# Optimization experiments

Measured on AMD Instinct MI355X. Metric: run time of the kernel, lower is better.

## Reference

```python
import jax, jax.numpy as jnp
import numpy as np

D_MODEL = 512
N_HEADS = 8
D_HEAD = D_MODEL // N_HEADS


def entmax15(z, axis=-1):
    """Exact sort-based entmax-1.5 along `axis` (Peters et al. 2019)."""
    z = jnp.moveaxis(z, axis, -1)
    x = z / 2.0
    x = x - jnp.max(x, axis=-1, keepdims=True)
    x_srt = -jnp.sort(-x, axis=-1)  # descending
    D = x_srt.shape[-1]
    k = jnp.arange(1, D + 1, dtype=x.dtype)
    cs = jnp.cumsum(x_srt, axis=-1)
    cs2 = jnp.cumsum(x_srt * x_srt, axis=-1)
    mean = cs / k
    ss = k * (cs2 / k - mean * mean)
    delta = (1.0 - ss) / k
    tau = mean - jnp.sqrt(jnp.clip(delta, 0.0))
    support = (tau <= x_srt).astype(jnp.int32)
    support_size = jnp.sum(support, axis=-1, keepdims=True)  # >= 1
    tau_star = jnp.take_along_axis(tau, support_size - 1, axis=-1)
    out = jnp.square(jnp.clip(x - tau_star, 0.0))
    return jnp.moveaxis(out, -1, axis)


def setup_inputs() -> dict:
    key = jax.random.key(0)
    ks = jax.random.split(key, 12)
    B, L = 8, 1024
    s = 1.0 / np.sqrt(D_MODEL)
    inp = {
        "query": jax.random.normal(ks[0], (B, L, D_MODEL), jnp.float32),
        "key": jax.random.normal(ks[1], (B, L, D_MODEL), jnp.float32),
        "value": jax.random.normal(ks[2], (B, L, D_MODEL), jnp.float32),
        "key_padding_mask": jnp.zeros((B, L), jnp.bool_),
        "q_w": jax.random.uniform(ks[3], (D_MODEL, D_MODEL), jnp.float32, -s, s),
        "q_b": jax.random.uniform(ks[4], (D_MODEL,), jnp.float32, -s, s),
        "k_w": jax.random.uniform(ks[5], (D_MODEL, D_MODEL), jnp.float32, -s, s),
        "k_b": jax.random.uniform(ks[6], (D_MODEL,), jnp.float32, -s, s),
        "v_w": jax.random.uniform(ks[7], (D_MODEL, D_MODEL), jnp.float32, -s, s),
        "v_b": jax.random.uniform(ks[8], (D_MODEL,), jnp.float32, -s, s),
        "out_w": jax.random.uniform(ks[9], (D_MODEL, D_MODEL), jnp.float32, -s, s),
        "out_b": jax.random.uniform(ks[10], (D_MODEL,), jnp.float32, -s, s),
    }
    return inp


def reference(query, key, value, key_padding_mask, q_w, q_b, k_w, k_b, v_w, v_b, out_w, out_b):
    B, L, _ = query.shape
    scale = D_HEAD ** -0.5
    # torch Linear: y = x @ W^T + b
    def split_heads(x):
        return x.reshape(B, L, N_HEADS, D_HEAD).transpose(0, 2, 1, 3)  # [B,H,L,d]
    q = split_heads(query @ q_w.T + q_b)
    k = split_heads(key @ k_w.T + k_b)
    v = split_heads(value @ v_w.T + v_b)
    scores = jnp.einsum('bhqd,bhkd->bhqk', q, k) * scale  # [B,H,L,L]
    mask = key_padding_mask[:, None, None, :]
    scores = jnp.where(mask, jnp.asarray(-1e9, scores.dtype), scores)
    attn = entmax15(scores, axis=-1)  # dropout in eval mode -> identity
    ctx = jnp.einsum('bhqk,bhkd->bhqd', attn, v)
    ctx = ctx.transpose(0, 2, 1, 3).reshape(B, L, D_MODEL)
    return ctx @ out_w.T + out_b
```

## Files before the change

kernel.cpp:

```cpp
#include <hip/hip_runtime.h>
#include <stdint.h>

typedef _Float16 f16;
typedef __attribute__((ext_vector_type(8))) f16 f16x8;
typedef __attribute__((ext_vector_type(2))) f16 h2;
typedef __attribute__((ext_vector_type(4))) float f32x4;
typedef unsigned short u16;
typedef unsigned int u32;
typedef unsigned char u8;

#define LL 1024
#define DM 512

__device__ __forceinline__ u16 f2h(float f){ return __builtin_bit_cast(u16, (f16)f); }
__device__ __forceinline__ u32 pack2(float a, float b){
  h2 v; v.x = (f16)a; v.y = (f16)b; return __builtin_bit_cast(u32, v);
}
__device__ __forceinline__ f32x4 mfma16h(f16x8 a, f16x8 b, f32x4 c){
  return __builtin_amdgcn_mfma_f32_16x16x32_f16(a, b, c, 0, 0, 0);
}

template<int CTRL>
__device__ __forceinline__ float dpp_mov(float x){
  return __builtin_bit_cast(float,
    __builtin_amdgcn_update_dpp(0, __builtin_bit_cast(int, x), CTRL, 0xF, 0xF, true));
}
__device__ __forceinline__ float red_add16(float v){
  v += dpp_mov<0x128>(v);
  v += dpp_mov<0x124>(v);
  v += dpp_mov<0x122>(v);
  v += dpp_mov<0x121>(v);
  return v;
}
__device__ __forceinline__ float red_max16(float v){
  v = fmaxf(v, dpp_mov<0x128>(v));
  v = fmaxf(v, dpp_mov<0x124>(v));
  v = fmaxf(v, dpp_mov<0x122>(v));
  v = fmaxf(v, dpp_mov<0x121>(v));
  return v;
}

struct CvtArgs {
  const float* src[7];
  u16* dst[7];
  int n4[7];
};

__global__ __launch_bounds__(256) void cvt_kernel(CvtArgs a){
  int seg = blockIdx.y;
  const float4* s = (const float4*)a.src[seg];
  ushort4* d = (ushort4*)a.dst[seg];
  int n4 = a.n4[seg];
  for (int i = blockIdx.x*blockDim.x + threadIdx.x; i < n4; i += gridDim.x*blockDim.x){
    float4 v = s[i];
    ushort4 o;
    o.x = f2h(v.x); o.y = f2h(v.y); o.z = f2h(v.z); o.w = f2h(v.w);
    d[i] = o;
  }
}

struct QkvArgs {
  const u16* A[3];
  const u16* W[3];
  const float* bias[3];
  u16* dst[3];
  float scale[3];
};

__global__ __launch_bounds__(256,2) void proj_qkv(QkvArgs args){
  __shared__ u16 SM[128*128];
  u16* As = SM;
  u16* Bs = SM + 128*64;
  const int tid = threadIdx.x;
  const int w = tid>>6, lane = tid&63;
  const int g = lane>>4, r16 = lane&15;
  const int wr = w>>1, wc = w&1;

  const int which = blockIdx.y>>2, nt = blockIdx.y&3;
  const bool isV = (which==2);
  const u16* A = args.A[which];
  const u16* W = args.W[which];
  const float* bias = args.bias[which];
  u16* dsth = args.dst[which];
  const float scale = args.scale[which];

  const int m0 = blockIdx.x*128, n0 = nt*128;

  f32x4 acc[4][4] = {};

  int rowc[4], slc[4];
  #pragma unroll
  for (int i=0;i<4;++i){
    int c = i*256+tid;
    rowc[i] = c>>3;
    slc[i] = (c&7) ^ ((c>>3)&7);
  }

  const int fswz = r16 & 7;

  for (int k0=0; k0<DM; k0+=64){
    #pragma unroll
    for (int i=0;i<4;++i){
      int c = i*256+tid;
      __builtin_amdgcn_global_load_lds(
        (const __attribute__((address_space(1))) void*)(A + (size_t)(m0+rowc[i])*DM + k0 + slc[i]*8),
        (__attribute__((address_space(3))) void*)(&As[c*8]), 16, 0, 0);
      __builtin_amdgcn_global_load_lds(
        (const __attribute__((address_space(1))) void*)(W + (size_t)(n0+rowc[i])*DM + k0 + slc[i]*8),
        (__attribute__((address_space(3))) void*)(&Bs[c*8]), 16, 0, 0);
    }
    __syncthreads();

    f16x8 af[4][2], bfr[4][2];
    #pragma unroll
    for (int mi=0; mi<4; ++mi){
      int row = wr*64 + mi*16 + r16;
      #pragma unroll
      for (int ks=0; ks<2; ++ks)
        af[mi][ks] = *(const f16x8*)(&As[row*64 + ((ks*4+g)^fswz)*8]);
    }
    #pragma unroll
    for (int ni=0; ni<4; ++ni){
      int row = wc*64 + ni*16 + r16;
      #pragma unroll
      for (int ks=0; ks<2; ++ks)
        bfr[ni][ks] = *(const f16x8*)(&Bs[row*64 + ((ks*4+g)^fswz)*8]);
    }
    if (isV){
      #pragma unroll
      for (int mi=0; mi<4; ++mi)
        #pragma unroll
        for (int ni=0; ni<4; ++ni){
          acc[mi][ni] = mfma16h(af[mi][0], bfr[ni][0], acc[mi][ni]);
          acc[mi][ni] = mfma16h(af[mi][1], bfr[ni][1], acc[mi][ni]);
        }
    } else {
      #pragma unroll
      for (int mi=0; mi<4; ++mi)
        #pragma unroll
        for (int ni=0; ni<4; ++ni){
          acc[mi][ni] = mfma16h(bfr[ni][0], af[mi][0], acc[mi][ni]);
          acc[mi][ni] = mfma16h(bfr[ni][1], af[mi][1], acc[mi][ni]);
        }
    }
    __syncthreads();
  }

  if (!isV){
    #pragma unroll
    for (int mi=0; mi<4; ++mi){
      #pragma unroll
      for (int ni=0; ni<4; ++ni){
        f32x4 a = acc[mi][ni];
        int row = wr*64 + mi*16 + r16;
        int c   = wc*16 + ni*4 + g;
        float4 bv = *(const float4*)(bias + n0 + c*4);
        uint2 pk;
        pk.x = pack2((a[0]+bv.x)*scale, (a[1]+bv.y)*scale);
        pk.y = pack2((a[2]+bv.z)*scale, (a[3]+bv.w)*scale);
        *(uint2*)(&SM[row*128 + ((c ^ ((row&7)<<2))<<2)]) = pk;
      }
    }
  } else {
    #pragma unroll
    for (int mi=0; mi<4; ++mi){
      #pragma unroll
      for (int ni=0; ni<4; ++ni){
        f32x4 a = acc[mi][ni];
        int fl = wc*64 + ni*16 + r16;
        int kc = wr*16 + mi*4 + g;
        float bv = bias[n0 + fl];
        uint2 pk;
        pk.x = pack2(a[0]+bv, a[1]+bv);
        pk.y = pack2(a[2]+bv, a[3]+bv);
        *(uint2*)(&SM[fl*128 + ((kc ^ ((fl&7)<<2))<<2)]) = pk;
      }
    }
  }
  __syncthreads();

  #pragma unroll
  for (int rr=0; rr<8; ++rr){
    int row = w*32 + rr*4 + (lane>>4);
    int c0 = (lane&15)*2;
    int cs = c0 ^ ((row&7)<<2);
    uint4 v = *(const uint4*)(&SM[row*128 + (cs<<2)]);
    if (!isV){
      *(uint4*)(dsth + (size_t)(m0+row)*DM + n0 + (c0<<2)) = v;
    } else {
      int n = n0 + row;
      int hh = n>>6, d = n&63, bb = m0>>10;
      *(uint4*)(dsth + (size_t)((bb*8+hh)*64 + d)*1024 + (m0&1023) + (c0<<2)) = v;
    }
  }
}

__global__ __launch_bounds__(256,2) void proj_out(
    const u16* __restrict__ A, const u16* __restrict__ W,
    const float* __restrict__ bias, float* __restrict__ dstf)
{
  __shared__ u16 As[64*64];
  __shared__ u16 Bs[128*64];
  const int tid = threadIdx.x;
  const int w = tid>>6, lane = tid&63;
  const int g = lane>>4, r16 = lane&15;
  const int m0 = blockIdx.x*64, n0 = blockIdx.y*128;

  f32x4 acc[4][2] = {};

  int rowa[2], slota[2];
  #pragma unroll
  for (int i=0;i<2;++i){ int c = i*256+tid; rowa[i]=c>>3; slota[i]=c&7; }
  int rowb[4], slotb[4];
  #pragma unroll
  for (int i=0;i<4;++i){ int c = i*256+tid; rowb[i]=c>>3; slotb[i]=c&7; }

  uint4 ra[2], rb[4];
  #pragma unroll
  for (int i=0;i<2;++i)
    ra[i] = *(const uint4*)(A + (size_t)(m0+rowa[i])*DM + slota[i]*8);
  #pragma unroll
  for (int i=0;i<4;++i)
    rb[i] = *(const uint4*)(W + (size_t)(n0+rowb[i])*DM + slotb[i]*8);

  const int fswz = r16 & 7;

  for (int k0=0; k0<DM; k0+=64){
    __syncthreads();
    #pragma unroll
    for (int i=0;i<2;++i)
      *(uint4*)(&As[rowa[i]*64 + (slota[i]^(rowa[i]&7))*8]) = ra[i];
    #pragma unroll
    for (int i=0;i<4;++i)
      *(uint4*)(&Bs[rowb[i]*64 + (slotb[i]^(rowb[i]&7))*8]) = rb[i];
    __syncthreads();
    int kn = (k0+64 < DM) ? (k0+64) : 0;
    #pragma unroll
    for (int i=0;i<2;++i)
      ra[i] = *(const uint4*)(A + (size_t)(m0+rowa[i])*DM + kn + slota[i]*8);
    #pragma unroll
    for (int i=0;i<4;++i)
      rb[i] = *(const uint4*)(W + (size_t)(n0+rowb[i])*DM + kn + slotb[i]*8);

    f16x8 af[4][2], bfr[2][2];
    #pragma unroll
    for (int mi=0; mi<4; ++mi){
      int row = mi*16 + r16;
      #pragma unroll
      for (int ks=0; ks<2; ++ks)
        af[mi][ks] = *(const f16x8*)(&As[row*64 + ((ks*4+g)^fswz)*8]);
    }
    #pragma unroll
    for (int ni=0; ni<2; ++ni){
      int row = w*32 + ni*16 + r16;
      #pragma unroll
      for (int ks=0; ks<2; ++ks)
        bfr[ni][ks] = *(const f16x8*)(&Bs[row*64 + ((ks*4+g)^fswz)*8]);
    }
    #pragma unroll
    for (int mi=0; mi<4; ++mi)
      #pragma unroll
      for (int ni=0; ni<2; ++ni){
        acc[mi][ni] = mfma16h(bfr[ni][0], af[mi][0], acc[mi][ni]);
        acc[mi][ni] = mfma16h(bfr[ni][1], af[mi][1], acc[mi][ni]);
      }
  }

  #pragma unroll
  for (int mi=0; mi<4; ++mi){
    #pragma unroll
    for (int ni=0; ni<2; ++ni){
      int m  = m0 + mi*16 + r16;
      int nb = n0 + w*32 + ni*16 + g*4;
      float4 bv = *(const float4*)(bias + nb);
      float4 o;
      o.x = acc[mi][ni][0]+bv.x; o.y = acc[mi][ni][1]+bv.y;
      o.z = acc[mi][ni][2]+bv.z; o.w = acc[mi][ni][3]+bv.w;
      *(float4*)(dstf + (size_t)m*DM + nb) = o;
    }
  }
}

__global__ __launch_bounds__(256,4) void attn_entmax(
    const u16* __restrict__ Qf, const u16* __restrict__ Kf,
    const u16* __restrict__ Vt, const u8* __restrict__ mask,
    u16* __restrict__ ctx)
{
  __shared__ u16 S[16*1024];

  const int tid = threadIdx.x, w = tid>>6, lane = tid&63;
  const int g = lane>>4, r16 = lane&15;
  const int bid = blockIdx.x;
  const int bh = ((bid&7)<<3) | ((bid>>3)&7);
  const int qb = bid>>6;
  const int b = bh>>3, h = bh&7;
  const int q0 = qb*16;
  const u16* Qb = Qf + ((size_t)(b*LL + q0))*DM + h*64;
  const u16* Kb = Kf + ((size_t)(b*LL))*DM + h*64;

  f16x8 qf0 = *(const f16x8*)(Qb + (size_t)r16*DM + g*8);
  f16x8 qf1 = *(const f16x8*)(Qb + (size_t)r16*DM + 32 + g*8);
  #pragma unroll
  for (int kt=0; kt<16; ++kt){
    int krow = w*256 + kt*16;
    const u16* kp = Kb + (size_t)(krow + r16)*DM + g*8;
    f16x8 kf0 = *(const f16x8*)(kp);
    f16x8 kf1 = *(const f16x8*)(kp + 32);
    f32x4 acc = {};
    acc = mfma16h(kf0, qf0, acc);
    acc = mfma16h(kf1, qf1, acc);
    int kb = krow + g*4;
    u32 m4 = *(const u32*)(mask + b*LL + kb);
    float v0 = (m4 & 0xFFu)       ? -30000.f : acc[0];
    float v1 = (m4 & 0xFF00u)     ? -30000.f : acc[1];
    float v2 = (m4 & 0xFF0000u)   ? -30000.f : acc[2];
    float v3 = (m4 & 0xFF000000u) ? -30000.f : acc[3];
    int cc = ((kb>>6)&7) ^ (r16&7);
    uint2 pk; pk.x = pack2(v0,v1); pk.y = pack2(v2,v3);
    *(uint2*)(&S[r16*LL + (kb ^ (cc<<3))]) = pk;
  }
  __syncthreads();

  {
    const int r = w*4 + g;
    const int ccb = (r16 ^ r) & 7;
    h2 zp[32];
    #pragma unroll
    for (int c=0;c<8;++c){
      uint4 v = *(const uint4*)(&S[r*LL + ((r16*64 + c*8) ^ (ccb<<3))]);
      zp[c*4+0] = __builtin_bit_cast(h2, v.x);
      zp[c*4+1] = __builtin_bit_cast(h2, v.y);
      zp[c*4+2] = __builtin_bit_cast(h2, v.z);
      zp[c*4+3] = __builtin_bit_cast(h2, v.w);
    }
    h2 m2 = zp[0];
    #pragma unroll
    for (int t=1;t<32;++t) m2 = __builtin_elementwise_max(m2, zp[t]);
    float mx = red_max16(fmaxf((float)m2.x, (float)m2.y));

    const h2 zero2 = (h2)(f16)0;
    float lo = mx - 1.0f, hi = mx, tau = mx - 0.5f;
    #pragma unroll 1
    for (int it=0; it<6; ++it){
      f16 th = (f16)tau;
      h2 t2; t2.x = th; t2.y = th;
      h2 s1a = zero2, s1b = zero2, s2a = zero2, s2b = zero2;
      #pragma unroll
      for (int t=0;t<32;t+=2){
        h2 d0 = __builtin_elementwise_max(zp[t]   - t2, zero2);
        h2 d1 = __builtin_elementwise_max(zp[t+1] - t2, zero2);
        s1a = s1a + d0;        s1b = s1b + d1;
        s2a = s2a + d0*d0;     s2b = s2b + d1*d1;
      }
      h2 s1h = s1a + s1b, s2h = s2a + s2b;
      float s1 = red_add16((float)s1h.x + (float)s1h.y);
      float s2 = red_add16((float)s2h.x + (float)s2h.y);
      if (s2 >= 1.0f) lo = tau; else hi = tau;
      float tn = tau + (s2 - 1.0f)/(2.0f*s1);
      tau = (tn >= lo && tn < hi) ? tn : 0.5f*(lo+hi);
    }

    {
      f16 th = (f16)tau;
      h2 t2; t2.x = th; t2.y = th;
      h2 psa = zero2, psb = zero2;
      #pragma unroll
      for (int t=0;t<32;t+=2){
        h2 d0 = __builtin_elementwise_max(zp[t]   - t2, zero2);
        h2 d1 = __builtin_elementwise_max(zp[t+1] - t2, zero2);
        h2 p0 = d0*d0, p1 = d1*d1;
        zp[t] = p0; zp[t+1] = p1;
        psa = psa + p0; psb = psb + p1;
      }
      h2 ps2 = psa + psb;
      float ps = red_add16((float)ps2.x + (float)ps2.y);
      f16 iv = (f16)(1.0f/ps);
      h2 i2; i2.x = iv; i2.y = iv;
      #pragma unroll
      for (int c=0;c<8;++c){
        uint4 v;
        v.x = __builtin_bit_cast(u32, (h2)(zp[c*4+0]*i2));
        v.y = __builtin_bit_cast(u32, (h2)(zp[c*4+1]*i2));
        v.z = __builtin_bit_cast(u32, (h2)(zp[c*4+2]*i2));
        v.w = __builtin_bit_cast(u32, (h2)(zp[c*4+3]*i2));
        *(uint4*)(&S[r*LL + ((r16*64 + c*8) ^ (ccb<<3))]) = v;
      }
    }
  }
  __syncthreads();

  const u16* vrow = Vt + (size_t)(bh*64 + w*16 + r16)*LL;
  f32x4 o0 = {}, o1 = {};
  const int prow = r16;
  #pragma unroll 8
  for (int kt=0; kt<32; ++kt){
    int k = kt*32 + g*8;
    int cc = ((k>>6)&7) ^ (prow&7);
    f16x8 pa = *(const f16x8*)(&S[prow*LL + (k ^ (cc<<3))]);
    f16x8 vb = *(const f16x8*)(vrow + k);
    if (kt & 1) o1 = mfma16h(pa, vb, o1);
    else        o0 = mfma16h(pa, vb, o0);
  }
  #pragma unroll
  for (int r=0;r<4;++r){
    int q = q0 + g*4 + r;
    ctx[(size_t)(b*LL + q)*DM + h*64 + w*16 + r16] = f2h(o0[r] + o1[r]);
  }
}

extern "C" void kernel_launch(void* const* d_in, const int* in_sizes, int n_in,
                              void* d_out, int out_size, void* d_ws, size_t ws_size,
                              hipStream_t stream) {
  const float* query = (const float*)d_in[0];
  const float* key   = (const float*)d_in[1];
  const float* value = (const float*)d_in[2];
  const u8*    maskp = (const u8*)d_in[3];
  const float* q_w = (const float*)d_in[4];
  const float* q_b = (const float*)d_in[5];
  const float* k_w = (const float*)d_in[6];
  const float* k_b = (const float*)d_in[7];
  const float* v_w = (const float*)d_in[8];
  const float* v_b = (const float*)d_in[9];
  const float* out_w = (const float*)d_in[10];
  const float* out_b = (const float*)d_in[11];
  float* out = (float*)d_out;

  u16* qx = (u16*)d_ws;
  u16* kx = qx + 4194304;
  u16* vx = kx + 4194304;
  u16* wq = vx + 4194304;
  u16* wk = wq + 262144;
  u16* wv = wk + 262144;
  u16* wo = wv + 262144;
  u16* Qbuf = wo + 262144;
  u16* Kbuf = Qbuf + 4194304;
  u16* Vt   = Kbuf + 4194304;
  u16* ctxb = Vt + 4194304;

  CvtArgs ca;
  ca.src[0]=query; ca.dst[0]=qx; ca.n4[0]=8*LL*DM/4;
  ca.src[1]=key;   ca.dst[1]=kx; ca.n4[1]=8*LL*DM/4;
  ca.src[2]=value; ca.dst[2]=vx; ca.n4[2]=8*LL*DM/4;
  ca.src[3]=q_w;   ca.dst[3]=wq; ca.n4[3]=DM*DM/4;
  ca.src[4]=k_w;   ca.dst[4]=wk; ca.n4[4]=DM*DM/4;
  ca.src[5]=v_w;   ca.dst[5]=wv; ca.n4[5]=DM*DM/4;
  ca.src[6]=out_w; ca.dst[6]=wo; ca.n4[6]=DM*DM/4;
  cvt_kernel<<<dim3(512,7),256,0,stream>>>(ca);

  QkvArgs qa;
  qa.A[0]=qx; qa.A[1]=kx; qa.A[2]=vx;
  qa.W[0]=wq; qa.W[1]=wk; qa.W[2]=wv;
  qa.bias[0]=q_b; qa.bias[1]=k_b; qa.bias[2]=v_b;
  qa.dst[0]=Qbuf; qa.dst[1]=Kbuf; qa.dst[2]=Vt;
  qa.scale[0]=0.0625f; qa.scale[1]=1.0f; qa.scale[2]=1.0f;

  proj_qkv<<<dim3(64,12),256,0,stream>>>(qa);

  attn_entmax<<<dim3(4096),256,0,stream>>>(Qbuf, Kbuf, Vt, maskp, ctxb);

  proj_out<<<dim3(128,4),256,0,stream>>>(ctxb, wo, out_b, out);
}
```

Measured before the change: 192.8 us.

## Process 32 query rows per attention block and prefetch K/V fragments

The attention kernel now handles 32 query rows per block with 8 waves, so each K fragment loaded from global memory feeds MFMAs for two query tiles instead of one. This halves redundant K and mask traffic per query. The QK and PV loops are also restructured into double-buffered register groups that prefetch the next K, P and V fragments ahead of the MFMAs. In exchange, LDS per block doubles to 64KB, which may cap resident blocks per CU. Register pressure also rises from the prefetch buffers.

Result: faster. 181.6 us (-5.8%).

```diff
diff --git a/kernel.cpp b/kernel.cpp
--- a/kernel.cpp
+++ b/kernel.cpp
@@ -281,12 +281,12 @@
   }
 }
 
-__global__ __launch_bounds__(256,4) void attn_entmax(
+__global__ __launch_bounds__(512,4) void attn_entmax(
     const u16* __restrict__ Qf, const u16* __restrict__ Kf,
     const u16* __restrict__ Vt, const u8* __restrict__ mask,
     u16* __restrict__ ctx)
 {
-  __shared__ u16 S[16*1024];
+  __shared__ u16 S[32*1024];
 
   const int tid = threadIdx.x, w = tid>>6, lane = tid&63;
   const int g = lane>>4, r16 = lane&15;
@@ -294,30 +294,58 @@
   const int bh = ((bid&7)<<3) | ((bid>>3)&7);
   const int qb = bid>>6;
   const int b = bh>>3, h = bh&7;
-  const int q0 = qb*16;
+  const int q0 = qb*32;
   const u16* Qb = Qf + ((size_t)(b*LL + q0))*DM + h*64;
   const u16* Kb = Kf + ((size_t)(b*LL))*DM + h*64;
 
-  f16x8 qf0 = *(const f16x8*)(Qb + (size_t)r16*DM + g*8);
-  f16x8 qf1 = *(const f16x8*)(Qb + (size_t)r16*DM + 32 + g*8);
-  #pragma unroll
-  for (int kt=0; kt<16; ++kt){
-    int krow = w*256 + kt*16;
-    const u16* kp = Kb + (size_t)(krow + r16)*DM + g*8;
-    f16x8 kf0 = *(const f16x8*)(kp);
-    f16x8 kf1 = *(const f16x8*)(kp + 32);
-    f32x4 acc = {};
-    acc = mfma16h(kf0, qf0, acc);
-    acc = mfma16h(kf1, qf1, acc);
-    int kb = krow + g*4;
-    u32 m4 = *(const u32*)(mask + b*LL + kb);
-    float v0 = (m4 & 0xFFu)       ? -30000.f : acc[0];
-    float v1 = (m4 & 0xFF00u)     ? -30000.f : acc[1];
-    float v2 = (m4 & 0xFF0000u)   ? -30000.f : acc[2];
-    float v3 = (m4 & 0xFF000000u) ? -30000.f : acc[3];
-    int cc = ((kb>>6)&7) ^ (r16&7);
-    uint2 pk; pk.x = pack2(v0,v1); pk.y = pack2(v2,v3);
-    *(uint2*)(&S[r16*LL + (kb ^ (cc<<3))]) = pk;
+  f16x8 qf[2][2];
+  #pragma unroll
+  for (int qi=0;qi<2;++qi){
+    qf[qi][0] = *(const f16x8*)(Qb + (size_t)(qi*16 + r16)*DM + g*8);
+    qf[qi][1] = *(const f16x8*)(Qb + (size_t)(qi*16 + r16)*DM + 32 + g*8);
+  }
+  {
+    f16x8 kc[2][2], kn[2][2];
+    #pragma unroll
+    for (int j=0;j<2;++j){
+      const u16* kp = Kb + (size_t)(w*128 + j*16 + r16)*DM + g*8;
+      kc[j][0] = *(const f16x8*)(kp);
+      kc[j][1] = *(const f16x8*)(kp + 32);
+    }
+    #pragma unroll
+    for (int grp=0; grp<4; ++grp){
+      #pragma unroll
+      for (int j=0;j<2;++j){
+        if (grp < 3){
+          const u16* kp = Kb + (size_t)(w*128 + (grp*2+2+j)*16 + r16)*DM + g*8;
+          kn[j][0] = *(const f16x8*)(kp);
+          kn[j][1] = *(const f16x8*)(kp + 32);
+        }
+      }
+      #pragma unroll
+      for (int j=0;j<2;++j){
+        int kt = grp*2 + j;
+        int krow = w*128 + kt*16;
+        int kb = krow + g*4;
+        u32 m4 = *(const u32*)(mask + b*LL + kb);
+        #pragma unroll
+        for (int qi=0; qi<2; ++qi){
+          f32x4 acc = {};
+          acc = mfma16h(kc[j][0], qf[qi][0], acc);
+          acc = mfma16h(kc[j][1], qf[qi][1], acc);
+          float v0 = (m4 & 0xFFu)       ? -30000.f : acc[0];
+          float v1 = (m4 & 0xFF00u)     ? -30000.f : acc[1];
+          float v2 = (m4 & 0xFF0000u)   ? -30000.f : acc[2];
+          float v3 = (m4 & 0xFF000000u) ? -30000.f : acc[3];
+          int row = qi*16 + r16;
+          int cc = ((kb>>6)&7) ^ (row&7);
+          uint2 pk; pk.x = pack2(v0,v1); pk.y = pack2(v2,v3);
+          *(uint2*)(&S[row*LL + (kb ^ (cc<<3))]) = pk;
+        }
+      }
+      #pragma unroll
+      for (int j=0;j<2;++j){ kc[j][0]=kn[j][0]; kc[j][1]=kn[j][1]; }
+    }
   }
   __syncthreads();
 
@@ -389,22 +417,43 @@
   }
   __syncthreads();
 
-  const u16* vrow = Vt + (size_t)(bh*64 + w*16 + r16)*LL;
+  const int qi = w>>2, di = w&3;
+  const u16* vrow = Vt + (size_t)(bh*64 + di*16 + r16)*LL;
+  const int prow = qi*16 + r16;
   f32x4 o0 = {}, o1 = {};
-  const int prow = r16;
-  #pragma unroll 8
-  for (int kt=0; kt<32; ++kt){
-    int k = kt*32 + g*8;
-    int cc = ((k>>6)&7) ^ (prow&7);
-    f16x8 pa = *(const f16x8*)(&S[prow*LL + (k ^ (cc<<3))]);
-    f16x8 vb = *(const f16x8*)(vrow + k);
-    if (kt & 1) o1 = mfma16h(pa, vb, o1);
-    else        o0 = mfma16h(pa, vb, o0);
+  {
+    f16x8 pc[4], vc[4], pn[4], vn[4];
+    #pragma unroll
+    for (int j=0;j<4;++j){
+      int k = j*32 + g*8;
+      int cc = ((k>>6)&7) ^ (prow&7);
+      pc[j] = *(const f16x8*)(&S[prow*LL + (k ^ (cc<<3))]);
+      vc[j] = *(const f16x8*)(vrow + k);
+    }
+    #pragma unroll
+    for (int grp=0; grp<8; ++grp){
+      #pragma unroll
+      for (int j=0;j<4;++j){
+        if (grp < 7){
+          int k = (grp*4+4+j)*32 + g*8;
+          int cc = ((k>>6)&7) ^ (prow&7);
+          pn[j] = *(const f16x8*)(&S[prow*LL + (k ^ (cc<<3))]);
+          vn[j] = *(const f16x8*)(vrow + k);
+        }
+      }
+      #pragma unroll
+      for (int j=0;j<4;++j){
+        if (j & 1) o1 = mfma16h(pc[j], vc[j], o1);
+        else       o0 = mfma16h(pc[j], vc[j], o0);
+      }
+      #pragma unroll
+      for (int j=0;j<4;++j){ pc[j]=pn[j]; vc[j]=vn[j]; }
+    }
   }
   #pragma unroll
   for (int r=0;r<4;++r){
-    int q = q0 + g*4 + r;
-    ctx[(size_t)(b*LL + q)*DM + h*64 + w*16 + r16] = f2h(o0[r] + o1[r]);
+    int q = q0 + qi*16 + g*4 + r;
+    ctx[(size_t)(b*LL + q)*DM + h*64 + di*16 + r16] = f2h(o0[r] + o1[r]);
   }
 }
 
@@ -456,7 +505,7 @@
 
   proj_qkv<<<dim3(64,12),256,0,stream>>>(qa);
 
-  attn_entmax<<<dim3(4096),256,0,stream>>>(Qbuf, Kbuf, Vt, maskp, ctxb);
+  attn_entmax<<<dim3(2048),512,0,stream>>>(Qbuf, Kbuf, Vt, maskp, ctxb);
 
   proj_out<<<dim3(128,4),256,0,stream>>>(ctxb, wo, out_b, out);
 }
```
